# Kernel optimization log

Hardware: AMD Instinct MI355X
Metric: run time of the kernel (lower is better)

## Reference

```python
import jax, jax.numpy as jnp
import numpy as np

LSTM_IN = 125
LSTM_H = 125
MLP_D_H = 512
N = 512


def _lstm_scan(x, Wih, Whh, bih, bhh):
    # x: (N, LSTM_IN); PyTorch gate order: i, f, g, o
    H = LSTM_H
    def step(carry, xt):
        h, c = carry
        g = Wih @ xt + Whh @ h + bih + bhh  # (4H,)
        i = jax.nn.sigmoid(g[:H])
        f = jax.nn.sigmoid(g[H:2 * H])
        gg = jnp.tanh(g[2 * H:3 * H])
        o = jax.nn.sigmoid(g[3 * H:])
        c = f * c + i * gg
        h = o * jnp.tanh(c)
        return (h, c), h
    init = (jnp.zeros((H,), x.dtype), jnp.zeros((H,), x.dtype))
    _, hs = jax.lax.scan(step, init, x)
    return hs  # (N, H)


def setup_inputs() -> dict:
    key = jax.random.key(0)
    ks = jax.random.split(key, 14)
    s = 0.05
    d = {
        "sentence_emb": jax.random.normal(ks[0], (N, 1, LSTM_IN), jnp.float32),
        "Wih_f": jax.random.normal(ks[1], (4 * LSTM_H, LSTM_IN), jnp.float32) * s,
        "Whh_f": jax.random.normal(ks[2], (4 * LSTM_H, LSTM_H), jnp.float32) * s,
        "bih_f": jax.random.normal(ks[3], (4 * LSTM_H,), jnp.float32) * s,
        "bhh_f": jax.random.normal(ks[4], (4 * LSTM_H,), jnp.float32) * s,
        "Wih_b": jax.random.normal(ks[5], (4 * LSTM_H, LSTM_IN), jnp.float32) * s,
        "Whh_b": jax.random.normal(ks[6], (4 * LSTM_H, LSTM_H), jnp.float32) * s,
        "bih_b": jax.random.normal(ks[7], (4 * LSTM_H,), jnp.float32) * s,
        "bhh_b": jax.random.normal(ks[8], (4 * LSTM_H,), jnp.float32) * s,
        "W1": jax.random.normal(ks[9], (MLP_D_H, 4 * LSTM_H), jnp.float32) * s,
        "b1": jax.random.normal(ks[10], (MLP_D_H,), jnp.float32) * s,
        "W2": jax.random.normal(ks[11], (1, MLP_D_H), jnp.float32) * s,
        "b2": jax.random.normal(ks[12], (1,), jnp.float32) * s,
    }
    return d


def reference(sentence_emb, Wih_f, Whh_f, bih_f, bhh_f, Wih_b, Whh_b, bih_b, bhh_b, W1, b1, W2, b2):
    x = sentence_emb[:, 0, :]  # (N, 125), batch=1
    h_fwd = _lstm_scan(x, Wih_f, Whh_f, bih_f, bhh_f)           # (N, 125)
    h_bwd = _lstm_scan(x[::-1], Wih_b, Whh_b, bih_b, bhh_b)[::-1]  # (N, 125)
    h = jnp.concatenate([h_fwd, h_bwd], axis=-1)  # (N, 250)
    # output_mtx[i, j] = MLP(concat(h[j], h[i]))
    # Decompose first linear: W1 @ cat(h_j, h_i) = Wa @ h_j + Wb @ h_i
    D = h.shape[-1]
    Pa = h @ W1[:, :D].T   # (N, H): contribution of h_j
    Pb = h @ W1[:, D:].T   # (N, H): contribution of h_i
    hidden = jnp.tanh(Pb[:, None, :] + Pa[None, :, :] + b1)  # (N, N, H)
    out = hidden @ W2[0] + b2[0]  # (N, N)
    return out
```

## Files before the change

### kernel.cpp

```cpp
#include <hip/hip_runtime.h>

typedef __bf16 bf16_t;
typedef __bf16 bf16x8 __attribute__((ext_vector_type(8)));
typedef float f32x4 __attribute__((ext_vector_type(4)));
typedef int   int4v __attribute__((ext_vector_type(4)));

#define LOG2E 1.4426950408889634f

template<int CTRL>
__device__ __forceinline__ float qperm(float x) {
  return __builtin_bit_cast(float,
      __builtin_amdgcn_update_dpp(0, __builtin_bit_cast(int, x), CTRL, 0xF, 0xF, true));
}

__device__ __forceinline__ void lds_barrier() {
  asm volatile("s_waitcnt lgkmcnt(0)\n\ts_barrier" ::: "memory");
}

__global__ __launch_bounds__(256) void pre_kernel(
    const float* __restrict__ x,
    const float* __restrict__ Wih_f, const float* __restrict__ bih_f,
    const float* __restrict__ bhh_f,
    const float* __restrict__ Wih_b, const float* __restrict__ bih_b,
    const float* __restrict__ bhh_b,
    float* __restrict__ preT)
{
  const int dir = blockIdx.x >> 5;
  const int T   = blockIdx.x & 31;
  const float* __restrict__ Wih = dir ? Wih_b : Wih_f;
  const float* __restrict__ bih = dir ? bih_b : bih_f;
  const float* __restrict__ bhh = dir ? bhh_b : bhh_f;

  const int tid = threadIdx.x;
  const int wv  = tid >> 6;
  const int lane = tid & 63;
  const int q = lane >> 4, cc = lane & 15;

  const int r  = 16 * T + cc;
  const int na = r >> 2, pa = r & 3;
  const bool vld = (na < 125);
  const float* __restrict__ Wr = Wih + (vld ? (125 * pa + na) * 125 : 0);

  bf16x8 whi[4], wlo[4];
  #pragma unroll
  for (int ks = 0; ks < 4; ++ks) {
    #pragma unroll
    for (int j = 0; j < 8; ++j) {
      int k = 32 * ks + 8 * q + j;
      float wvv = (vld && k < 125) ? Wr[k] : 0.0f;
      bf16_t hi = (bf16_t)wvv;
      whi[ks][j] = hi;
      wlo[ks][j] = (bf16_t)(wvv - (float)hi);
    }
  }

  float bias[4];
  #pragma unroll
  for (int reg = 0; reg < 4; ++reg) {
    int ro = 16 * T + 4 * q + reg;
    int no = ro >> 2, po = ro & 3;
    bias[reg] = (no < 125) ? (bih[125 * po + no] + bhh[125 * po + no]) : 0.0f;
  }

  for (int i = 0; i < 8; ++i) {
    const int tt = 8 * wv + i;
    const int t  = 16 * tt + cc;
    const int trow = dir ? (511 - t) : t;
    const float* __restrict__ xr = x + trow * 125;

    f32x4 acc = (f32x4)0.0f;
    #pragma unroll
    for (int ks = 0; ks < 4; ++ks) {
      bf16x8 xhi, xlo;
      #pragma unroll
      for (int j = 0; j < 8; ++j) {
        int k = 32 * ks + 8 * q + j;
        float xv = (k < 125) ? xr[k] : 0.0f;
        bf16_t hi = (bf16_t)xv;
        xhi[j] = hi;
        xlo[j] = (bf16_t)(xv - (float)hi);
      }
      acc = __builtin_amdgcn_mfma_f32_16x16x32_bf16(whi[ks], xhi, acc, 0, 0, 0);
      acc = __builtin_amdgcn_mfma_f32_16x16x32_bf16(whi[ks], xlo, acc, 0, 0, 0);
      acc = __builtin_amdgcn_mfma_f32_16x16x32_bf16(wlo[ks], xhi, acc, 0, 0, 0);
    }
    #pragma unroll
    for (int reg = 0; reg < 4; ++reg) {
      int ro = 16 * T + 4 * q + reg;
      preT[dir * 262144 + ro * 512 + 16 * tt + cc] = acc[reg] + bias[reg];
    }
  }
}

__global__ __launch_bounds__(512) void lstm_kernel(
    const float* __restrict__ Whh_f, const float* __restrict__ Whh_b,
    const float* __restrict__ pre,
    bf16_t* __restrict__ h_all)
{
  const int dir = blockIdx.x;
  const float* __restrict__ Whh = dir ? Whh_b : Whh_f;

  const int tid  = threadIdx.x;
  const int lane = tid & 63;
  const int w    = tid >> 6;
  const int q    = lane >> 4;
  const int cc   = lane & 15;
  const int lt   = cc >> 2;
  const int p    = cc & 3;

  float wm = 0.0f;
  #pragma unroll
  for (int LT = 0; LT < 4; ++LT) {
    int rr = 16 * (4 * w + LT) + cc;
    int nn = rr >> 2, pp = rr & 3;
    if (nn < 125) {
      const float* __restrict__ Wrow = Whh + (125 * pp + nn) * 125;
      #pragma unroll
      for (int ks = 0; ks < 2; ++ks)
        #pragma unroll
        for (int jj = 0; jj < 16; ++jj) {
          int k = 64 * ks + 16 * q + jj;
          if (k < 125) wm = fmaxf(wm, fabsf(Wrow[k]));
        }
    }
  }
  #pragma unroll
  for (int off = 1; off < 64; off <<= 1)
    wm = fmaxf(wm, __shfl_xor(wm, off));
  __shared__ float wmx[8];
  if (lane == 0) wmx[w] = wm;
  __syncthreads();
  float wmax = wmx[0];
  #pragma unroll
  for (int u = 1; u < 8; ++u) wmax = fmaxf(wmax, wmx[u]);
  const float s_w  = 127.0f / wmax;
  const float invq = wmax / (127.0f * 127.0f);

  int4v afrag[4][2];
  #pragma unroll
  for (int LT = 0; LT < 4; ++LT) {
    int rr = 16 * (4 * w + LT) + cc;
    int nn = rr >> 2, pp = rr & 3;
    bool avld = (nn < 125);
    const float* __restrict__ Wrow = Whh + (avld ? (125 * pp + nn) * 125 : 0);
    #pragma unroll
    for (int ks = 0; ks < 2; ++ks) {
      int4v v;
      #pragma unroll
      for (int word = 0; word < 4; ++word) {
        int b = 0;
        #pragma unroll
        for (int byte = 0; byte < 4; ++byte) {
          int jj = 4 * word + byte;
          int k  = 64 * ks + 16 * q + jj;
          int qv = 0;
          if (avld && k < 125)
            qv = (int)__builtin_rintf(Wrow[k] * s_w);
          b |= (qv & 0xFF) << (8 * byte);
        }
        v[word] = b;
      }
      afrag[LT][ks] = v;
    }
  }

  __shared__ __align__(16) char hbuf[2][128];
  if (tid < 256) hbuf[tid >> 7][tid & 127] = 0;
  if (dir == 0) {
    #pragma unroll
    for (int u = 0; u < 6; ++u) h_all[tid * 256 + 250 + u] = (bf16_t)0.0f;
  }
  __syncthreads();

  const int   r_lane = 64 * w + 16 * lt + 4 * q + p;
  const int   nset   = 16 * w + 4 * lt + q;
  const float mult   = (p == 2) ? (-2.0f * LOG2E) : (-LOG2E);
  const float sA     = (p == 2) ? 2.0f : 1.0f;
  const float sB     = (p == 2) ? -1.0f : 0.0f;
  const float dscale = mult * invq;
  const float* __restrict__ preR = pre + dir * 262144 + r_lane * 512;
  float c = 0.0f;

  float4 pv_cur = *(const float4*)preR;

  for (int g = 0; g < 128; ++g) {
    float4 pv_nxt = make_float4(0.f, 0.f, 0.f, 0.f);
    if (g < 127) pv_nxt = *(const float4*)(preR + 4 * (g + 1));

    #pragma unroll
    for (int s4 = 0; s4 < 4; ++s4) {
      const int step = 4 * g + s4;
      const int cur  = s4 & 1, nxt = cur ^ 1;
      const float pv = (s4 == 0) ? pv_cur.x : (s4 == 1) ? pv_cur.y
                     : (s4 == 2) ? pv_cur.z : pv_cur.w;
      const float pvm = mult * pv;

      int4v b0 = *(const int4v*)&hbuf[cur][16 * q];
      int4v b1 = *(const int4v*)&hbuf[cur][64 + 16 * q];

      int4v acc[4];
      #pragma unroll
      for (int LT = 0; LT < 4; ++LT) {
        int4v a = (int4v)0;
        a = __builtin_amdgcn_mfma_i32_16x16x64_i8(afrag[LT][0], b0, a, 0, 0, 0);
        a = __builtin_amdgcn_mfma_i32_16x16x64_i8(afrag[LT][1], b1, a, 0, 0, 0);
        acc[LT] = a;
      }

      int gl[4];
      #pragma unroll
      for (int LT = 0; LT < 4; ++LT) {
        int a01 = (p & 1) ? acc[LT][1] : acc[LT][0];
        int a23 = (p & 1) ? acc[LT][3] : acc[LT][2];
        gl[LT] = (p & 2) ? a23 : a01;
      }
      int b01 = (lt & 1) ? gl[1] : gl[0];
      int b23 = (lt & 1) ? gl[3] : gl[2];
      int gsel = (lt & 2) ? b23 : b01;

      float gf  = (float)gsel;
      float xg  = fmaf(gf, dscale, pvm);
      float e   = __builtin_amdgcn_exp2f(xg);
      float y   = __builtin_amdgcn_rcpf(1.0f + e);
      float act = fmaf(y, sA, sB);

      float b_i = qperm<0x00>(act);
      float b_f = qperm<0x55>(act);
      float b_g = qperm<0xAA>(act);
      float b_o = qperm<0xFF>(act);
      c = fmaf(b_f, c, b_i * b_g);
      float e2 = __builtin_amdgcn_exp2f(-2.0f * LOG2E * c);
      float tc = fmaf(__builtin_amdgcn_rcpf(1.0f + e2), 2.0f, -1.0f);
      float h  = b_o * tc;

      if (p == 0) {
        int qh = (int)__builtin_rintf(h * 127.0f);
        hbuf[nxt][nset] = (char)qh;
        if (nset < 125) {
          int t_orig = dir ? (511 - step) : step;
          h_all[t_orig * 256 + dir * 125 + nset] = (bf16_t)h;
        }
      }
      lds_barrier();
    }
    pv_cur = pv_nxt;
  }
}

__global__ __launch_bounds__(256) void qgemm_kernel(
    const bf16_t* __restrict__ h_all,
    const float* __restrict__ W1,
    const float* __restrict__ b1,
    float* __restrict__ Qa,
    float* __restrict__ Qb)
{
  const int tid  = threadIdx.x;
  const int wv   = tid >> 6;
  const int lane = tid & 63;
  const int q    = lane >> 4, cc = lane & 15;
  const int bj   = blockIdx.x & 31;
  const int bm   = blockIdx.x >> 5;
  const int m    = bm * 64 + wv * 16 + cc;
  const int j0   = bj * 16;
  const int jA   = j0 + cc;

  const bool isB = (m >= 512);
  const int  row = isB ? (m - 512) : m;
  const int  cof = isB ? 250 : 0;

  f32x4 acc = (f32x4)0.0f;
  #pragma unroll
  for (int ks = 0; ks < 8; ++ks) {
    int kb = 32 * ks + 8 * q;
    bf16x8 a = *(const bf16x8*)&h_all[jA * 256 + kb];
    bf16x8 b;
    #pragma unroll
    for (int jj = 0; jj < 8; ++jj) {
      int k = kb + jj;
      float v = (k < 250) ? W1[row * 500 + cof + k] : 0.0f;
      b[jj] = (bf16_t)v;
    }
    acc = __builtin_amdgcn_mfma_f32_16x16x32_bf16(a, b, acc, 0, 0, 0);
  }

  const float C2 = 2.0f * LOG2E;
  #pragma unroll
  for (int reg = 0; reg < 4; ++reg) {
    int j = j0 + 4 * q + reg;
    float v = acc[reg];
    if (!isB) Qa[j * 512 + m] = C2 * v;
    else      Qb[j * 512 + (m - 512)] = C2 * (v + b1[m - 512]);
  }
}

__global__ __launch_bounds__(256) void outer_kernel(
    const float* __restrict__ Qa, const float* __restrict__ Qb,
    const float* __restrict__ W2, const float* __restrict__ b2,
    float* __restrict__ out)
{
  __shared__ float sa[2][32][33];
  __shared__ float sb[2][32][33];
  __shared__ float sw[2][32];

  const int tid = threadIdx.x;
  const int bi  = blockIdx.x >> 4, bjx = blockIdx.x & 15;
  const int i0  = bi * 32, j0 = bjx * 32;
  const int ii0 = (tid & 15) * 2;
  const int jj0 = (tid >> 4) * 2;
  const int ljj = tid & 31, kk4 = (tid >> 5) * 4;

  float accR[2][2] = {{0.0f, 0.0f}, {0.0f, 0.0f}};
  float wsum = 0.0f;

  for (int kc = 0; kc < 16; ++kc) {
    const int buf = kc & 1;
    const int k0  = kc * 32;
    float4 va = *(const float4*)&Qa[(j0 + ljj) * 512 + k0 + kk4];
    float4 vb = *(const float4*)&Qb[(i0 + ljj) * 512 + k0 + kk4];
    sa[buf][kk4 + 0][ljj] = va.x; sa[buf][kk4 + 1][ljj] = va.y;
    sa[buf][kk4 + 2][ljj] = va.z; sa[buf][kk4 + 3][ljj] = va.w;
    sb[buf][kk4 + 0][ljj] = vb.x; sb[buf][kk4 + 1][ljj] = vb.y;
    sb[buf][kk4 + 2][ljj] = vb.z; sb[buf][kk4 + 3][ljj] = vb.w;
    if (tid < 32) sw[buf][tid] = W2[k0 + tid];
    __syncthreads();

    #pragma unroll 4
    for (int kk = 0; kk < 32; ++kk) {
      float2 av = *(const float2*)&sa[buf][kk][jj0];
      float2 bv = *(const float2*)&sb[buf][kk][ii0];
      float wk = sw[buf][kk];
      wsum += wk;
      {
        float e = __builtin_amdgcn_exp2f(av.x + bv.x);
        accR[0][0] = fmaf(wk, __builtin_amdgcn_rcpf(1.0f + e), accR[0][0]);
      }
      {
        float e = __builtin_amdgcn_exp2f(av.y + bv.x);
        accR[0][1] = fmaf(wk, __builtin_amdgcn_rcpf(1.0f + e), accR[0][1]);
      }
      {
        float e = __builtin_amdgcn_exp2f(av.x + bv.y);
        accR[1][0] = fmaf(wk, __builtin_amdgcn_rcpf(1.0f + e), accR[1][0]);
      }
      {
        float e = __builtin_amdgcn_exp2f(av.y + bv.y);
        accR[1][1] = fmaf(wk, __builtin_amdgcn_rcpf(1.0f + e), accR[1][1]);
      }
    }
  }

  const float bb = b2[0];
  #pragma unroll
  for (int i2 = 0; i2 < 2; ++i2)
    #pragma unroll
    for (int j2 = 0; j2 < 2; ++j2)
      out[(i0 + ii0 + i2) * 512 + (j0 + jj0 + j2)] =
          wsum - 2.0f * accR[i2][j2] + bb;
}

extern "C" void kernel_launch(void* const* d_in, const int* in_sizes, int n_in,
                              void* d_out, int out_size, void* d_ws, size_t ws_size,
                              hipStream_t stream) {
  const float* emb   = (const float*)d_in[0];
  const float* Wih_f = (const float*)d_in[1];
  const float* Whh_f = (const float*)d_in[2];
  const float* bih_f = (const float*)d_in[3];
  const float* bhh_f = (const float*)d_in[4];
  const float* Wih_b = (const float*)d_in[5];
  const float* Whh_b = (const float*)d_in[6];
  const float* bih_b = (const float*)d_in[7];
  const float* bhh_b = (const float*)d_in[8];
  const float* W1    = (const float*)d_in[9];
  const float* b1    = (const float*)d_in[10];
  const float* W2    = (const float*)d_in[11];
  const float* b2    = (const float*)d_in[12];
  float* out = (float*)d_out;

  char* ws = (char*)d_ws;
  float*  pre   = (float*)ws;
  bf16_t* h_all = (bf16_t*)(ws + 2 * 1024 * 1024);
  float*  Qa    = (float*)(ws + 2 * 1024 * 1024 + 256 * 1024);
  float*  Qb    = Qa + 512 * 512;

  pre_kernel<<<64, 256, 0, stream>>>(emb, Wih_f, bih_f, bhh_f,
                                     Wih_b, bih_b, bhh_b, pre);
  lstm_kernel<<<2, 512, 0, stream>>>(Whh_f, Whh_b, pre, h_all);
  qgemm_kernel<<<512, 256, 0, stream>>>(h_all, W1, b1, Qa, Qb);
  outer_kernel<<<256, 256, 0, stream>>>(Qa, Qb, W2, b2, out);
}
```

Before: 336.4 us.

## Halve LSTM block waves with two rows per lane; split-K outer kernel with atomics

The LSTM recurrence kernel now runs 4 waves per block instead of 8. Each lane handles two hidden units, so there are twice as many MFMAs per wave but fewer waves taking part in each per-step barrier, which targets the latency of the serial loop. The outer tanh-MLP kernel splits the reduction dimension in two, launches twice as many blocks, and accumulates into a zeroed output with atomicAdd. This adds a memset and atomic traffic, and makes the floating-point summation order depend on timing.

```diff
diff --git a/kernel.cpp b/kernel.cpp
--- a/kernel.cpp
+++ b/kernel.cpp
@@ -92,7 +92,7 @@
   }
 }
 
-__global__ __launch_bounds__(512) void lstm_kernel(
+__global__ __launch_bounds__(256, 1) void lstm_kernel(
     const float* __restrict__ Whh_f, const float* __restrict__ Whh_b,
     const float* __restrict__ pre,
     bf16_t* __restrict__ h_all)
@@ -110,8 +110,8 @@
 
   float wm = 0.0f;
   #pragma unroll
-  for (int LT = 0; LT < 4; ++LT) {
-    int rr = 16 * (4 * w + LT) + cc;
+  for (int LT = 0; LT < 8; ++LT) {
+    int rr = 16 * (8 * w + LT) + cc;
     int nn = rr >> 2, pp = rr & 3;
     if (nn < 125) {
       const float* __restrict__ Wrow = Whh + (125 * pp + nn) * 125;
@@ -127,19 +127,17 @@
   #pragma unroll
   for (int off = 1; off < 64; off <<= 1)
     wm = fmaxf(wm, __shfl_xor(wm, off));
-  __shared__ float wmx[8];
+  __shared__ float wmx[4];
   if (lane == 0) wmx[w] = wm;
   __syncthreads();
-  float wmax = wmx[0];
-  #pragma unroll
-  for (int u = 1; u < 8; ++u) wmax = fmaxf(wmax, wmx[u]);
+  float wmax = fmaxf(fmaxf(wmx[0], wmx[1]), fmaxf(wmx[2], wmx[3]));
   const float s_w  = 127.0f / wmax;
   const float invq = wmax / (127.0f * 127.0f);
 
-  int4v afrag[4][2];
-  #pragma unroll
-  for (int LT = 0; LT < 4; ++LT) {
-    int rr = 16 * (4 * w + LT) + cc;
+  int4v afrag[8][2];
+  #pragma unroll
+  for (int LT = 0; LT < 8; ++LT) {
+    int rr = 16 * (8 * w + LT) + cc;
     int nn = rr >> 2, pp = rr & 3;
     bool avld = (nn < 125);
     const float* __restrict__ Wrow = Whh + (avld ? (125 * pp + nn) * 125 : 0);
@@ -165,85 +163,109 @@
   }
 
   __shared__ __align__(16) char hbuf[2][128];
-  if (tid < 256) hbuf[tid >> 7][tid & 127] = 0;
+  hbuf[tid >> 7][tid & 127] = 0;
   if (dir == 0) {
     #pragma unroll
-    for (int u = 0; u < 6; ++u) h_all[tid * 256 + 250 + u] = (bf16_t)0.0f;
+    for (int rr = 0; rr < 2; ++rr)
+      #pragma unroll
+      for (int u = 0; u < 6; ++u)
+        h_all[(tid + 256 * rr) * 256 + 250 + u] = (bf16_t)0.0f;
   }
   __syncthreads();
 
-  const int   r_lane = 64 * w + 16 * lt + 4 * q + p;
-  const int   nset   = 16 * w + 4 * lt + q;
+  const int   r0  = 128 * w + 16 * lt + 4 * q + p;
+  const int   r1  = r0 + 64;
+  const int   n0  = 32 * w + 4 * lt + q;
+  const int   n1  = n0 + 16;
   const float mult   = (p == 2) ? (-2.0f * LOG2E) : (-LOG2E);
   const float sA     = (p == 2) ? 2.0f : 1.0f;
   const float sB     = (p == 2) ? -1.0f : 0.0f;
   const float dscale = mult * invq;
-  const float* __restrict__ preR = pre + dir * 262144 + r_lane * 512;
-  float c = 0.0f;
-
-  float4 pv_cur = *(const float4*)preR;
+  const float* __restrict__ preR0 = pre + dir * 262144 + r0 * 512;
+  const float* __restrict__ preR1 = pre + dir * 262144 + r1 * 512;
+  float c0 = 0.0f, c1 = 0.0f;
+
+  float4 pv0_cur = *(const float4*)preR0;
+  float4 pv1_cur = *(const float4*)preR1;
 
   for (int g = 0; g < 128; ++g) {
-    float4 pv_nxt = make_float4(0.f, 0.f, 0.f, 0.f);
-    if (g < 127) pv_nxt = *(const float4*)(preR + 4 * (g + 1));
+    float4 pv0_nxt = make_float4(0.f, 0.f, 0.f, 0.f);
+    float4 pv1_nxt = pv0_nxt;
+    if (g < 127) {
+      pv0_nxt = *(const float4*)(preR0 + 4 * (g + 1));
+      pv1_nxt = *(const float4*)(preR1 + 4 * (g + 1));
+    }
 
     #pragma unroll
     for (int s4 = 0; s4 < 4; ++s4) {
       const int step = 4 * g + s4;
       const int cur  = s4 & 1, nxt = cur ^ 1;
-      const float pv = (s4 == 0) ? pv_cur.x : (s4 == 1) ? pv_cur.y
-                     : (s4 == 2) ? pv_cur.z : pv_cur.w;
-      const float pvm = mult * pv;
+      const float pv0 = (s4 == 0) ? pv0_cur.x : (s4 == 1) ? pv0_cur.y
+                      : (s4 == 2) ? pv0_cur.z : pv0_cur.w;
+      const float pv1 = (s4 == 0) ? pv1_cur.x : (s4 == 1) ? pv1_cur.y
+                      : (s4 == 2) ? pv1_cur.z : pv1_cur.w;
+      const float pvm0 = mult * pv0;
+      const float pvm1 = mult * pv1;
 
       int4v b0 = *(const int4v*)&hbuf[cur][16 * q];
       int4v b1 = *(const int4v*)&hbuf[cur][64 + 16 * q];
 
-      int4v acc[4];
+      int4v acc[8];
       #pragma unroll
-      for (int LT = 0; LT < 4; ++LT) {
+      for (int LT = 0; LT < 8; ++LT) {
         int4v a = (int4v)0;
         a = __builtin_amdgcn_mfma_i32_16x16x64_i8(afrag[LT][0], b0, a, 0, 0, 0);
         a = __builtin_amdgcn_mfma_i32_16x16x64_i8(afrag[LT][1], b1, a, 0, 0, 0);
         acc[LT] = a;
       }
 
-      int gl[4];
-      #pragma unroll
-      for (int LT = 0; LT < 4; ++LT) {
-        int a01 = (p & 1) ? acc[LT][1] : acc[LT][0];
-        int a23 = (p & 1) ? acc[LT][3] : acc[LT][2];
-        gl[LT] = (p & 2) ? a23 : a01;
-      }
-      int b01 = (lt & 1) ? gl[1] : gl[0];
-      int b23 = (lt & 1) ? gl[3] : gl[2];
-      int gsel = (lt & 2) ? b23 : b01;
-
-      float gf  = (float)gsel;
-      float xg  = fmaf(gf, dscale, pvm);
-      float e   = __builtin_amdgcn_exp2f(xg);
-      float y   = __builtin_amdgcn_rcpf(1.0f + e);
-      float act = fmaf(y, sA, sB);
-
-      float b_i = qperm<0x00>(act);
-      float b_f = qperm<0x55>(act);
-      float b_g = qperm<0xAA>(act);
-      float b_o = qperm<0xFF>(act);
-      c = fmaf(b_f, c, b_i * b_g);
-      float e2 = __builtin_amdgcn_exp2f(-2.0f * LOG2E * c);
-      float tc = fmaf(__builtin_amdgcn_rcpf(1.0f + e2), 2.0f, -1.0f);
-      float h  = b_o * tc;
+      int4v v01  = (lt & 1) ? acc[1] : acc[0];
+      int4v v23  = (lt & 1) ? acc[3] : acc[2];
+      int4v vA   = (lt & 2) ? v23 : v01;
+      int4v v45  = (lt & 1) ? acc[5] : acc[4];
+      int4v v67  = (lt & 1) ? acc[7] : acc[6];
+      int4v vB   = (lt & 2) ? v67 : v45;
+      int a01 = (p & 1) ? vA[1] : vA[0];
+      int a23 = (p & 1) ? vA[3] : vA[2];
+      int gsel0 = (p & 2) ? a23 : a01;
+      int b01v = (p & 1) ? vB[1] : vB[0];
+      int b23v = (p & 1) ? vB[3] : vB[2];
+      int gsel1 = (p & 2) ? b23v : b01v;
+
+      float xg0 = fmaf((float)gsel0, dscale, pvm0);
+      float xg1 = fmaf((float)gsel1, dscale, pvm1);
+      float e0  = __builtin_amdgcn_exp2f(xg0);
+      float e1  = __builtin_amdgcn_exp2f(xg1);
+      float y0  = __builtin_amdgcn_rcpf(1.0f + e0);
+      float y1  = __builtin_amdgcn_rcpf(1.0f + e1);
+      float act0 = fmaf(y0, sA, sB);
+      float act1 = fmaf(y1, sA, sB);
+
+      float i0v = qperm<0x00>(act0), f0v = qperm<0x55>(act0);
+      float g0v = qperm<0xAA>(act0), o0v = qperm<0xFF>(act0);
+      float i1v = qperm<0x00>(act1), f1v = qperm<0x55>(act1);
+      float g1v = qperm<0xAA>(act1), o1v = qperm<0xFF>(act1);
+      c0 = fmaf(f0v, c0, i0v * g0v);
+      c1 = fmaf(f1v, c1, i1v * g1v);
+      float ec0 = __builtin_amdgcn_exp2f(-2.0f * LOG2E * c0);
+      float ec1 = __builtin_amdgcn_exp2f(-2.0f * LOG2E * c1);
+      float tc0 = fmaf(__builtin_amdgcn_rcpf(1.0f + ec0), 2.0f, -1.0f);
+      float tc1 = fmaf(__builtin_amdgcn_rcpf(1.0f + ec1), 2.0f, -1.0f);
+      float h0 = o0v * tc0;
+      float h1 = o1v * tc1;
 
       if (p == 0) {
-        int qh = (int)__builtin_rintf(h * 127.0f);
-        hbuf[nxt][nset] = (char)qh;
-        if (nset < 125) {
-          int t_orig = dir ? (511 - step) : step;
-          h_all[t_orig * 256 + dir * 125 + nset] = (bf16_t)h;
-        }
+        hbuf[nxt][n0] = (char)(int)__builtin_rintf(h0 * 127.0f);
+        hbuf[nxt][n1] = (char)(int)__builtin_rintf(h1 * 127.0f);
+        int t_orig = dir ? (511 - step) : step;
+        h_all[t_orig * 256 + dir * 125 + n0] = (bf16_t)h0;
+        if (n1 < 125)
+          h_all[t_orig * 256 + dir * 125 + n1] = (bf16_t)h1;
       }
       lds_barrier();
     }
-    pv_cur = pv_nxt;
+    pv0_cur = pv0_nxt;
+    pv1_cur = pv1_nxt;
   }
 }
 
@@ -302,19 +324,22 @@
   __shared__ float sb[2][32][33];
   __shared__ float sw[2][32];
 
-  const int tid = threadIdx.x;
-  const int bi  = blockIdx.x >> 4, bjx = blockIdx.x & 15;
-  const int i0  = bi * 32, j0 = bjx * 32;
-  const int ii0 = (tid & 15) * 2;
-  const int jj0 = (tid >> 4) * 2;
-  const int ljj = tid & 31, kk4 = (tid >> 5) * 4;
+  const int tid  = threadIdx.x;
+  const int bk   = blockIdx.x >> 8;
+  const int tile = blockIdx.x & 255;
+  const int bi   = tile >> 4, bjx = tile & 15;
+  const int i0   = bi * 32, j0 = bjx * 32;
+  const int ii0  = (tid & 15) * 2;
+  const int jj0  = (tid >> 4) * 2;
+  const int ljj  = tid & 31, kk4 = (tid >> 5) * 4;
+  const int kbase = bk * 256;
 
   float accR[2][2] = {{0.0f, 0.0f}, {0.0f, 0.0f}};
   float wsum = 0.0f;
 
-  for (int kc = 0; kc < 16; ++kc) {
+  for (int kc = 0; kc < 8; ++kc) {
     const int buf = kc & 1;
-    const int k0  = kc * 32;
+    const int k0  = kbase + kc * 32;
     float4 va = *(const float4*)&Qa[(j0 + ljj) * 512 + k0 + kk4];
     float4 vb = *(const float4*)&Qb[(i0 + ljj) * 512 + k0 + kk4];
     sa[buf][kk4 + 0][ljj] = va.x; sa[buf][kk4 + 1][ljj] = va.y;
@@ -349,13 +374,13 @@
     }
   }
 
-  const float bb = b2[0];
+  const float bb = (bk == 0) ? b2[0] : 0.0f;
   #pragma unroll
   for (int i2 = 0; i2 < 2; ++i2)
     #pragma unroll
     for (int j2 = 0; j2 < 2; ++j2)
-      out[(i0 + ii0 + i2) * 512 + (j0 + jj0 + j2)] =
-          wsum - 2.0f * accR[i2][j2] + bb;
+      atomicAdd(&out[(i0 + ii0 + i2) * 512 + (j0 + jj0 + j2)],
+                wsum - 2.0f * accR[i2][j2] + bb);
 }
 
 extern "C" void kernel_launch(void* const* d_in, const int* in_sizes, int n_in,
@@ -384,7 +409,8 @@
 
   pre_kernel<<<64, 256, 0, stream>>>(emb, Wih_f, bih_f, bhh_f,
                                      Wih_b, bih_b, bhh_b, pre);
-  lstm_kernel<<<2, 512, 0, stream>>>(Whh_f, Whh_b, pre, h_all);
+  lstm_kernel<<<2, 256, 0, stream>>>(Whh_f, Whh_b, pre, h_all);
   qgemm_kernel<<<512, 256, 0, stream>>>(h_all, W1, b1, Qa, Qb);
-  outer_kernel<<<256, 256, 0, stream>>>(Qa, Qb, W2, b2, out);
-}
+  hipMemsetAsync(out, 0, (size_t)out_size * sizeof(float), stream);
+  outer_kernel<<<512, 256, 0, stream>>>(Qa, Qb, W2, b2, out);
+}
```

New measurement: 379.7 us. +12.9%, slower.

## Spread LSTM recurrence over 16 waves and split-K the outer kernel

Applied to the files above, without the earlier changes.

The recurrent LSTM kernel now runs with 1024 threads, so each wave computes two 16-row MFMA tiles instead of four. This shortens the per-step chain of dependent int8 MFMAs and simplifies gate selection, at the cost of a 16-wave barrier every step. Separately, the outer tanh-MLP kernel splits the 512-wide hidden reduction into two halves across 512 blocks. The halves are combined with atomicAdd into an output zeroed by a memset, which adds a memset launch and atomic traffic in exchange for more parallel blocks.

```diff
diff --git a/kernel.cpp b/kernel.cpp
--- a/kernel.cpp
+++ b/kernel.cpp
@@ -92,7 +92,7 @@
   }
 }
 
-__global__ __launch_bounds__(512) void lstm_kernel(
+__global__ __launch_bounds__(1024, 4) void lstm_kernel(
     const float* __restrict__ Whh_f, const float* __restrict__ Whh_b,
     const float* __restrict__ pre,
     bf16_t* __restrict__ h_all)
@@ -107,11 +107,12 @@
   const int cc   = lane & 15;
   const int lt   = cc >> 2;
   const int p    = cc & 3;
+  const int ltp  = lt & 1;
 
   float wm = 0.0f;
   #pragma unroll
-  for (int LT = 0; LT < 4; ++LT) {
-    int rr = 16 * (4 * w + LT) + cc;
+  for (int LT = 0; LT < 2; ++LT) {
+    int rr = 16 * (2 * w + LT) + cc;
     int nn = rr >> 2, pp = rr & 3;
     if (nn < 125) {
       const float* __restrict__ Wrow = Whh + (125 * pp + nn) * 125;
@@ -127,19 +128,19 @@
   #pragma unroll
   for (int off = 1; off < 64; off <<= 1)
     wm = fmaxf(wm, __shfl_xor(wm, off));
-  __shared__ float wmx[8];
+  __shared__ float wmx[16];
   if (lane == 0) wmx[w] = wm;
   __syncthreads();
   float wmax = wmx[0];
   #pragma unroll
-  for (int u = 1; u < 8; ++u) wmax = fmaxf(wmax, wmx[u]);
+  for (int u = 1; u < 16; ++u) wmax = fmaxf(wmax, wmx[u]);
   const float s_w  = 127.0f / wmax;
   const float invq = wmax / (127.0f * 127.0f);
 
-  int4v afrag[4][2];
-  #pragma unroll
-  for (int LT = 0; LT < 4; ++LT) {
-    int rr = 16 * (4 * w + LT) + cc;
+  int4v afrag[2][2];
+  #pragma unroll
+  for (int LT = 0; LT < 2; ++LT) {
+    int rr = 16 * (2 * w + LT) + cc;
     int nn = rr >> 2, pp = rr & 3;
     bool avld = (nn < 125);
     const float* __restrict__ Wrow = Whh + (avld ? (125 * pp + nn) * 125 : 0);
@@ -166,14 +167,15 @@
 
   __shared__ __align__(16) char hbuf[2][128];
   if (tid < 256) hbuf[tid >> 7][tid & 127] = 0;
-  if (dir == 0) {
-    #pragma unroll
-    for (int u = 0; u < 6; ++u) h_all[tid * 256 + 250 + u] = (bf16_t)0.0f;
+  if (dir == 0 && tid < 512) {
+    #pragma unroll
+    for (int u = 0; u < 6; ++u)
+      h_all[tid * 256 + 250 + u] = (bf16_t)0.0f;
   }
   __syncthreads();
 
-  const int   r_lane = 64 * w + 16 * lt + 4 * q + p;
-  const int   nset   = 16 * w + 4 * lt + q;
+  const int   r_lane = 32 * w + 16 * ltp + 4 * q + p;
+  const int   n0     = 8 * w + 4 * ltp + q;
   const float mult   = (p == 2) ? (-2.0f * LOG2E) : (-LOG2E);
   const float sA     = (p == 2) ? 2.0f : 1.0f;
   const float sB     = (p == 2) ? -1.0f : 0.0f;
@@ -198,28 +200,21 @@
       int4v b0 = *(const int4v*)&hbuf[cur][16 * q];
       int4v b1 = *(const int4v*)&hbuf[cur][64 + 16 * q];
 
-      int4v acc[4];
+      int4v a0 = (int4v)0;
+      a0 = __builtin_amdgcn_mfma_i32_16x16x64_i8(afrag[0][0], b0, a0, 0, 0, 0);
+      a0 = __builtin_amdgcn_mfma_i32_16x16x64_i8(afrag[0][1], b1, a0, 0, 0, 0);
+      int4v a1 = (int4v)0;
+      a1 = __builtin_amdgcn_mfma_i32_16x16x64_i8(afrag[1][0], b0, a1, 0, 0, 0);
+      a1 = __builtin_amdgcn_mfma_i32_16x16x64_i8(afrag[1][1], b1, a1, 0, 0, 0);
+
+      int4v vA;
       #pragma unroll
-      for (int LT = 0; LT < 4; ++LT) {
-        int4v a = (int4v)0;
-        a = __builtin_amdgcn_mfma_i32_16x16x64_i8(afrag[LT][0], b0, a, 0, 0, 0);
-        a = __builtin_amdgcn_mfma_i32_16x16x64_i8(afrag[LT][1], b1, a, 0, 0, 0);
-        acc[LT] = a;
-      }
-
-      int gl[4];
-      #pragma unroll
-      for (int LT = 0; LT < 4; ++LT) {
-        int a01 = (p & 1) ? acc[LT][1] : acc[LT][0];
-        int a23 = (p & 1) ? acc[LT][3] : acc[LT][2];
-        gl[LT] = (p & 2) ? a23 : a01;
-      }
-      int b01 = (lt & 1) ? gl[1] : gl[0];
-      int b23 = (lt & 1) ? gl[3] : gl[2];
-      int gsel = (lt & 2) ? b23 : b01;
-
-      float gf  = (float)gsel;
-      float xg  = fmaf(gf, dscale, pvm);
+      for (int i = 0; i < 4; ++i) vA[i] = ltp ? a1[i] : a0[i];
+      int a01 = (p & 1) ? vA[1] : vA[0];
+      int a23 = (p & 1) ? vA[3] : vA[2];
+      int gsel = (p & 2) ? a23 : a01;
+
+      float xg  = fmaf((float)gsel, dscale, pvm);
       float e   = __builtin_amdgcn_exp2f(xg);
       float y   = __builtin_amdgcn_rcpf(1.0f + e);
       float act = fmaf(y, sA, sB);
@@ -233,12 +228,11 @@
       float tc = fmaf(__builtin_amdgcn_rcpf(1.0f + e2), 2.0f, -1.0f);
       float h  = b_o * tc;
 
-      if (p == 0) {
-        int qh = (int)__builtin_rintf(h * 127.0f);
-        hbuf[nxt][nset] = (char)qh;
-        if (nset < 125) {
+      if (p == 0 && lt < 2) {
+        hbuf[nxt][n0] = (char)(int)__builtin_rintf(h * 127.0f);
+        if (n0 < 125) {
           int t_orig = dir ? (511 - step) : step;
-          h_all[t_orig * 256 + dir * 125 + nset] = (bf16_t)h;
+          h_all[t_orig * 256 + dir * 125 + n0] = (bf16_t)h;
         }
       }
       lds_barrier();
@@ -302,19 +296,22 @@
   __shared__ float sb[2][32][33];
   __shared__ float sw[2][32];
 
-  const int tid = threadIdx.x;
-  const int bi  = blockIdx.x >> 4, bjx = blockIdx.x & 15;
-  const int i0  = bi * 32, j0 = bjx * 32;
-  const int ii0 = (tid & 15) * 2;
-  const int jj0 = (tid >> 4) * 2;
-  const int ljj = tid & 31, kk4 = (tid >> 5) * 4;
+  const int tid  = threadIdx.x;
+  const int bk   = blockIdx.x >> 8;
+  const int tile = blockIdx.x & 255;
+  const int bi   = tile >> 4, bjx = tile & 15;
+  const int i0   = bi * 32, j0 = bjx * 32;
+  const int ii0  = (tid & 15) * 2;
+  const int jj0  = (tid >> 4) * 2;
+  const int ljj  = tid & 31, kk4 = (tid >> 5) * 4;
+  const int kbase = bk * 256;
 
   float accR[2][2] = {{0.0f, 0.0f}, {0.0f, 0.0f}};
   float wsum = 0.0f;
 
-  for (int kc = 0; kc < 16; ++kc) {
+  for (int kc = 0; kc < 8; ++kc) {
     const int buf = kc & 1;
-    const int k0  = kc * 32;
+    const int k0  = kbase + kc * 32;
     float4 va = *(const float4*)&Qa[(j0 + ljj) * 512 + k0 + kk4];
     float4 vb = *(const float4*)&Qb[(i0 + ljj) * 512 + k0 + kk4];
     sa[buf][kk4 + 0][ljj] = va.x; sa[buf][kk4 + 1][ljj] = va.y;
@@ -349,13 +346,13 @@
     }
   }
 
-  const float bb = b2[0];
+  const float bb = (bk == 0) ? b2[0] : 0.0f;
   #pragma unroll
   for (int i2 = 0; i2 < 2; ++i2)
     #pragma unroll
     for (int j2 = 0; j2 < 2; ++j2)
-      out[(i0 + ii0 + i2) * 512 + (j0 + jj0 + j2)] =
-          wsum - 2.0f * accR[i2][j2] + bb;
+      atomicAdd(&out[(i0 + ii0 + i2) * 512 + (j0 + jj0 + j2)],
+                wsum - 2.0f * accR[i2][j2] + bb);
 }
 
 extern "C" void kernel_launch(void* const* d_in, const int* in_sizes, int n_in,
@@ -384,7 +381,8 @@
 
   pre_kernel<<<64, 256, 0, stream>>>(emb, Wih_f, bih_f, bhh_f,
                                      Wih_b, bih_b, bhh_b, pre);
-  lstm_kernel<<<2, 512, 0, stream>>>(Whh_f, Whh_b, pre, h_all);
+  lstm_kernel<<<2, 1024, 0, stream>>>(Whh_f, Whh_b, pre, h_all);
   qgemm_kernel<<<512, 256, 0, stream>>>(h_all, W1, b1, Qa, Qb);
-  outer_kernel<<<256, 256, 0, stream>>>(Qa, Qb, W2, b2, out);
-}
+  hipMemsetAsync(out, 0, (size_t)out_size * sizeof(float), stream);
+  outer_kernel<<<512, 256, 0, stream>>>(Qa, Qb, W2, b2, out);
+}
```

Result: slower. 355.8 us (+5.8%).
